# Optimization experiments

Hardware: AMD Instinct MI355X
Metric: run time of the kernel (lower is better)

The kernel has to match this reference:

```python
import jax, jax.numpy as jnp
import numpy as np

B, T, H = 16384, 64, 8
VOCABS = [2, 2, 21, 22, 5, 2, 22, 24]
EDIMS = [1, 1, 3, 3, 1, 1, 3, 3]


def _lstm_layer(xs, W_ih, W_hh, b_ih, b_hh):
    # xs: [B, T, F] -> hidden sequence [B, T, H]; torch gate order (i, f, g, o)
    Bsz = xs.shape[0]
    Hd = W_hh.shape[1]

    def step(carry, x_t):
        h, c = carry
        gates = x_t @ W_ih.T + b_ih + h @ W_hh.T + b_hh  # [B, 4H]
        i, f, g, o = jnp.split(gates, 4, axis=-1)
        c = jax.nn.sigmoid(f) * c + jax.nn.sigmoid(i) * jnp.tanh(g)
        h = jax.nn.sigmoid(o) * jnp.tanh(c)
        return (h, c), h

    init = (jnp.zeros((Bsz, Hd), xs.dtype), jnp.zeros((Bsz, Hd), xs.dtype))
    _, hs = jax.lax.scan(step, init, jnp.swapaxes(xs, 0, 1))  # scan over time
    return jnp.swapaxes(hs, 0, 1)


def setup_inputs() -> dict:
    key = jax.random.key(0)
    ks = jax.random.split(key, 40)
    cols = [jax.random.randint(ks[i], (B, T, 1), 0, VOCABS[i], dtype=jnp.int32) for i in range(8)]
    x = jnp.concatenate(cols, axis=2)  # [B, T, 8] categorical ids

    def p(k, shape):
        return jax.random.normal(k, shape, jnp.float32) * 0.1

    d = {"x": x}
    for i in range(8):
        d["e" + str(i + 1)] = p(ks[8 + i], (VOCABS[i], EDIMS[i]))
    d["W_ih0"] = p(ks[16], (4 * H, 16)); d["W_hh0"] = p(ks[17], (4 * H, H))
    d["b_ih0"] = p(ks[18], (4 * H,));   d["b_hh0"] = p(ks[19], (4 * H,))
    d["W_ih1"] = p(ks[20], (4 * H, H)); d["W_hh1"] = p(ks[21], (4 * H, H))
    d["b_ih1"] = p(ks[22], (4 * H,));   d["b_hh1"] = p(ks[23], (4 * H,))
    d["fc6_w"] = p(ks[24], (4, H)); d["fc6_b"] = p(ks[25], (4,))
    d["fc7_w"] = p(ks[26], (1, 4)); d["fc7_b"] = p(ks[27], (1,))
    d["fc1_w"] = p(ks[28], (4, H)); d["fc1_b"] = p(ks[29], (4,))
    d["fc2_w"] = p(ks[30], (1, 4)); d["fc2_b"] = p(ks[31], (1,))
    d["fc3_w"] = p(ks[32], (1, T)); d["fc3_b"] = p(ks[33], (1,))
    return d


def reference(x, e1, e2, e3, e4, e5, e6, e7, e8,
              W_ih0, W_hh0, b_ih0, b_hh0, W_ih1, W_hh1, b_ih1, b_hh1,
              fc6_w, fc6_b, fc7_w, fc7_b, fc1_w, fc1_b, fc2_w, fc2_b, fc3_w, fc3_b):
    tabs = (e1, e2, e3, e4, e5, e6, e7, e8)
    # 8-way embedding lookup + concat -> [B, T, 16]
    emb = jnp.concatenate([tabs[i][x[:, :, i]] for i in range(8)], axis=2)
    h1 = _lstm_layer(emb, W_ih0, W_hh0, b_ih0, b_hh0)
    out = _lstm_layer(h1, W_ih1, W_hh1, b_ih1, b_hh1)  # [B, T, H]
    # tiny dual FC branches applied per (b, t) position
    theta = ((out @ fc6_w.T + fc6_b) @ fc7_w.T + fc7_b)[..., 0]  # [B, T]
    h = ((out @ fc1_w.T + fc1_b) @ fc2_w.T + fc2_b)[..., 0]      # [B, T]
    pred = (theta * h) @ fc3_w.T + fc3_b  # [B, 1]
    return pred
```

## Files before the change

### kernel.cpp

```cpp
#include <hip/hip_runtime.h>
#include <hip/hip_bf16.h>

typedef float f2 __attribute__((ext_vector_type(2)));

__device__ __forceinline__ float sigf(float x) {
  return __builtin_amdgcn_rcpf(1.0f + __expf(-x));
}
__device__ __forceinline__ float tanh_fast(float x) {
  return fmaf(-2.0f, __builtin_amdgcn_rcpf(1.0f + __expf(2.0f * x)), 1.0f);
}

template<int CTRL>
__device__ __forceinline__ float dppf(float v) {
  return __builtin_bit_cast(float,
      __builtin_amdgcn_mov_dpp(__builtin_bit_cast(int, v), CTRL, 0xf, 0xf, false));
}

__device__ __forceinline__ void fanout8(float h, float* d) {
  d[0] = h;
  d[1] = dppf<0xB1>(h);
  d[2] = dppf<0x4E>(h);
  d[3] = dppf<0x1B>(h);
  float t7 = dppf<0x141>(h);
  d[7] = t7;
  d[4] = dppf<0x1B>(t7);
  d[5] = dppf<0x4E>(t7);
  d[6] = dppf<0xB1>(t7);
}

__launch_bounds__(256, 2)
__global__ void lstm_fused(
    const int* __restrict__ x,
    const float* __restrict__ e1, const float* __restrict__ e2,
    const float* __restrict__ e3, const float* __restrict__ e4,
    const float* __restrict__ e5, const float* __restrict__ e6,
    const float* __restrict__ e7, const float* __restrict__ e8,
    const float* __restrict__ W_ih0, const float* __restrict__ W_hh0,
    const float* __restrict__ b_ih0, const float* __restrict__ b_hh0,
    const float* __restrict__ W_ih1, const float* __restrict__ W_hh1,
    const float* __restrict__ b_ih1, const float* __restrict__ b_hh1,
    const float* __restrict__ fc6_w, const float* __restrict__ fc6_b,
    const float* __restrict__ fc7_w, const float* __restrict__ fc7_b,
    const float* __restrict__ fc1_w, const float* __restrict__ fc1_b,
    const float* __restrict__ fc2_w, const float* __restrict__ fc2_b,
    const float* __restrict__ fc3_w, const float* __restrict__ fc3_b,
    float* __restrict__ out)
{
  __shared__ __align__(16) float sTf[3200];
  __shared__ float sW3s[65];

  const int tid = threadIdx.x;

  {
    constexpr int RO[8]  = {0,2,4,25,47,52,54,76};
    constexpr int ED[8]  = {1,1,3,3,1,1,3,3};
    constexpr int CO[8]  = {0,1,2,5,8,9,10,13};
    constexpr int VOC[8] = {2,2,21,22,5,2,22,24};
    const float* ep[8] = {e1,e2,e3,e4,e5,e6,e7,e8};
    #pragma unroll
    for (int f = 0; f < 8; ++f) {
      const float* E = ep[f];
      for (int idx = tid; idx < VOC[f]*32; idx += 256) {
        int v = idx >> 5, m = idx & 31;
        int jj = m >> 2, q = m & 3, g = q*8 + jj;
        float s = 0.0f;
        #pragma unroll
        for (int d = 0; d < ED[f]; ++d)
          s += E[v*ED[f]+d] * W_ih0[g*16 + CO[f] + d];
        if (f == 0) s += b_ih0[g] + b_hh0[g];
        sTf[(RO[f]+v)*32 + m] = s;
      }
    }
    if (tid < 64) sW3s[tid+1] = fc3_w[tid];
    if (tid == 64) sW3s[0] = 0.f;
  }
  __syncthreads();

  const int j = tid & 7;
  const int b = (blockIdx.x << 5) + (tid >> 3);

  f2 wIF0[8], wGO0[8], iIF1[8], iGO1[8], rIF1[8], rGO1[8];
  #pragma unroll
  for (int r = 0; r < 8; ++r) {
    const int k = j ^ r;
    wIF0[r] = (f2){W_hh0[(0*8+j)*8+k], W_hh0[(1*8+j)*8+k]};
    wGO0[r] = (f2){W_hh0[(2*8+j)*8+k], W_hh0[(3*8+j)*8+k]};
    iIF1[r] = (f2){W_ih1[(0*8+j)*8+k], W_ih1[(1*8+j)*8+k]};
    iGO1[r] = (f2){W_ih1[(2*8+j)*8+k], W_ih1[(3*8+j)*8+k]};
    rIF1[r] = (f2){W_hh1[(0*8+j)*8+k], W_hh1[(1*8+j)*8+k]};
    rGO1[r] = (f2){W_hh1[(2*8+j)*8+k], W_hh1[(3*8+j)*8+k]};
  }
  const f2 bIF1 = {b_ih1[j]    + b_hh1[j],    b_ih1[8+j]  + b_hh1[8+j]};
  const f2 bGO1 = {b_ih1[16+j] + b_hh1[16+j], b_ih1[24+j] + b_hh1[24+j]};

  float f7[4], f2c[4];
  #pragma unroll
  for (int q = 0; q < 4; ++q) { f7[q] = fc7_w[q]; f2c[q] = fc2_w[q]; }
  f2 uvk[8];
  #pragma unroll
  for (int r = 0; r < 8; ++r) {
    const int k = j ^ r;
    float s1 = 0.f, s2 = 0.f;
    #pragma unroll
    for (int q = 0; q < 4; ++q) {
      s1 += f7[q]  * fc6_w[q*8+k];
      s2 += f2c[q] * fc1_w[q*8+k];
    }
    uvk[r] = (f2){s1, s2};
  }
  float cth = fc7_b[0], chh = fc2_b[0];
  #pragma unroll
  for (int q = 0; q < 4; ++q) { cth += f7[q]*fc6_b[q]; chh += f2c[q]*fc1_b[q]; }
  const f2 cc = {cth, chh};
  const float fc3b = fc3_b[0];

  float h0x[8], h1x[8];
  #pragma unroll
  for (int k = 0; k < 8; ++k) { h0x[k] = 0.f; h1x[k] = 0.f; }
  float c0 = 0.f, c1 = 0.f, acc = 0.f;

  const int4* xp = (const int4*)(x + (size_t)b * 512);
  const float4* tf4 = (const float4*)sTf;

  int4 ia = xp[0], ib = xp[1];
  float4 G0 = tf4[(      ia.x)*8 + j];
  float4 G1 = tf4[(  2 + ia.y)*8 + j];
  float4 G2 = tf4[(  4 + ia.z)*8 + j];
  float4 G3 = tf4[( 25 + ia.w)*8 + j];
  float4 G4 = tf4[( 47 + ib.x)*8 + j];
  float4 G5 = tf4[( 52 + ib.y)*8 + j];
  float4 G6 = tf4[( 54 + ib.z)*8 + j];
  float4 G7 = tf4[( 76 + ib.w)*8 + j];
  int4 na = xp[2], nb = xp[3];

  #pragma unroll 1
  for (int t = 0; t < 64; ++t) {
    const float w3p = sW3s[t];

    f2 sIFa = ((f2){G0.x,G0.y} + (f2){G1.x,G1.y}) + ((f2){G2.x,G2.y} + (f2){G3.x,G3.y});
    f2 sIFb = ((f2){G4.x,G4.y} + (f2){G5.x,G5.y}) + ((f2){G6.x,G6.y} + (f2){G7.x,G7.y});
    f2 sGOa = ((f2){G0.z,G0.w} + (f2){G1.z,G1.w}) + ((f2){G2.z,G2.w} + (f2){G3.z,G3.w});
    f2 sGOb = ((f2){G4.z,G4.w} + (f2){G5.z,G5.w}) + ((f2){G6.z,G6.w} + (f2){G7.z,G7.w});

    G0 = tf4[(      na.x)*8 + j];
    G1 = tf4[(  2 + na.y)*8 + j];
    G2 = tf4[(  4 + na.z)*8 + j];
    G3 = tf4[( 25 + na.w)*8 + j];
    G4 = tf4[( 47 + nb.x)*8 + j];
    G5 = tf4[( 52 + nb.y)*8 + j];
    G6 = tf4[( 54 + nb.z)*8 + j];
    G7 = tf4[( 76 + nb.w)*8 + j];

    {
      const int tn = (2*t + 4 <= 126) ? (2*t + 4) : 126;
      na = xp[tn]; nb = xp[tn+1];
    }

    f2 GIFa = bIF1, GIFb = (f2){0.f,0.f}, GGOa = bGO1, GGOb = (f2){0.f,0.f};
    f2 thfa = cc,  thfb = (f2){0.f,0.f};
    #pragma unroll
    for (int r = 0; r < 8; r += 2) {
      f2 hA = (f2)(h1x[r]), hB = (f2)(h1x[r+1]);
      GIFa = __builtin_elementwise_fma(rIF1[r],   hA, GIFa);
      GIFb = __builtin_elementwise_fma(rIF1[r+1], hB, GIFb);
      GGOa = __builtin_elementwise_fma(rGO1[r],   hA, GGOa);
      GGOb = __builtin_elementwise_fma(rGO1[r+1], hB, GGOb);
      thfa = __builtin_elementwise_fma(uvk[r],    hA, thfa);
      thfb = __builtin_elementwise_fma(uvk[r+1],  hB, thfb);
    }
    f2 thf = thfa + thfb;
    acc = fmaf(thf.x * thf.y, w3p, acc);

    #pragma unroll
    for (int r = 0; r < 8; r += 2) {
      sIFa = __builtin_elementwise_fma(wIF0[r],   (f2)(h0x[r]),   sIFa);
      sIFb = __builtin_elementwise_fma(wIF0[r+1], (f2)(h0x[r+1]), sIFb);
      sGOa = __builtin_elementwise_fma(wGO0[r],   (f2)(h0x[r]),   sGOa);
      sGOb = __builtin_elementwise_fma(wGO0[r+1], (f2)(h0x[r+1]), sGOb);
    }
    f2 gIF = sIFa + sIFb, gGO = sGOa + sGOb;
    float si = sigf(gIF.x), sf = sigf(gIF.y), tg = tanh_fast(gGO.x), so = sigf(gGO.y);
    c0 = fmaf(sf, c0, si * tg);
    float h0 = so * tanh_fast(c0);

    fanout8(h0, h0x);

    #pragma unroll
    for (int r = 0; r < 8; r += 2) {
      GIFa = __builtin_elementwise_fma(iIF1[r],   (f2)(h0x[r]),   GIFa);
      GIFb = __builtin_elementwise_fma(iIF1[r+1], (f2)(h0x[r+1]), GIFb);
      GGOa = __builtin_elementwise_fma(iGO1[r],   (f2)(h0x[r]),   GGOa);
      GGOb = __builtin_elementwise_fma(iGO1[r+1], (f2)(h0x[r+1]), GGOb);
    }
    f2 GIF = GIFa + GIFb, GGO = GGOa + GGOb;
    float si1 = sigf(GIF.x), sf1 = sigf(GIF.y), tg1 = tanh_fast(GGO.x), so1 = sigf(GGO.y);
    c1 = fmaf(sf1, c1, si1 * tg1);
    float h1 = so1 * tanh_fast(c1);

    fanout8(h1, h1x);
  }

  {
    f2 thfa = cc, thfb = (f2){0.f,0.f};
    #pragma unroll
    for (int r = 0; r < 8; r += 2) {
      thfa = __builtin_elementwise_fma(uvk[r],   (f2)(h1x[r]),   thfa);
      thfb = __builtin_elementwise_fma(uvk[r+1], (f2)(h1x[r+1]), thfb);
    }
    f2 thf = thfa + thfb;
    acc = fmaf(thf.x * thf.y, sW3s[64], acc);
  }

  if (j == 0) out[b] = acc + fc3b;
}

extern "C" void kernel_launch(void* const* d_in, const int* in_sizes, int n_in,
                              void* d_out, int out_size, void* d_ws, size_t ws_size,
                              hipStream_t stream) {
  const int* x = (const int*)d_in[0];
  const float *E1=(const float*)d_in[1],  *E2=(const float*)d_in[2],
              *E3=(const float*)d_in[3],  *E4=(const float*)d_in[4],
              *E5=(const float*)d_in[5],  *E6=(const float*)d_in[6],
              *E7=(const float*)d_in[7],  *E8=(const float*)d_in[8];
  const float *Wih0=(const float*)d_in[9],  *Whh0=(const float*)d_in[10],
              *bih0=(const float*)d_in[11], *bhh0=(const float*)d_in[12],
              *Wih1=(const float*)d_in[13], *Whh1=(const float*)d_in[14],
              *bih1=(const float*)d_in[15], *bhh1=(const float*)d_in[16],
              *fc6w=(const float*)d_in[17], *fc6b=(const float*)d_in[18],
              *fc7w=(const float*)d_in[19], *fc7b=(const float*)d_in[20],
              *fc1w=(const float*)d_in[21], *fc1b=(const float*)d_in[22],
              *fc2w=(const float*)d_in[23], *fc2b=(const float*)d_in[24],
              *fc3w=(const float*)d_in[25], *fc3b=(const float*)d_in[26];

  lstm_fused<<<512, 256, 0, stream>>>(
      x, E1,E2,E3,E4,E5,E6,E7,E8,
      Wih0, Whh0, bih0, bhh0, Wih1, Whh1, bih1, bhh1,
      fc6w, fc6b, fc7w, fc7b, fc1w, fc1b, fc2w, fc2b, fc3w, fc3b,
      (float*)d_out);
}
```

Baseline: 179.7 us.

## Split each LSTM row across 16 lanes with two gates per lane

Each batch row now uses 16 threads instead of 8, so each lane computes two gate pre-activations instead of four. Hidden-state broadcast moves from DPP fanout to shared-memory writes and reads. Embedding tables for paired binary features are merged into combined rows, cutting the per-step LDS lookups. The grid doubles and launch bounds allow more blocks per CU, which adds latency hiding but relies on implicit wave-synchronous LDS ordering without barriers and adds more LDS traffic per step.

```diff
diff --git a/kernel.cpp b/kernel.cpp
--- a/kernel.cpp
+++ b/kernel.cpp
@@ -9,27 +9,14 @@
 __device__ __forceinline__ float tanh_fast(float x) {
   return fmaf(-2.0f, __builtin_amdgcn_rcpf(1.0f + __expf(2.0f * x)), 1.0f);
 }
-
 template<int CTRL>
 __device__ __forceinline__ float dppf(float v) {
   return __builtin_bit_cast(float,
       __builtin_amdgcn_mov_dpp(__builtin_bit_cast(int, v), CTRL, 0xf, 0xf, false));
 }
 
-__device__ __forceinline__ void fanout8(float h, float* d) {
-  d[0] = h;
-  d[1] = dppf<0xB1>(h);
-  d[2] = dppf<0x4E>(h);
-  d[3] = dppf<0x1B>(h);
-  float t7 = dppf<0x141>(h);
-  d[7] = t7;
-  d[4] = dppf<0x1B>(t7);
-  d[5] = dppf<0x4E>(t7);
-  d[6] = dppf<0xB1>(t7);
-}
-
-__launch_bounds__(256, 2)
-__global__ void lstm_fused(
+__launch_bounds__(256, 4)
+__global__ void lstm_fused16(
     const int* __restrict__ x,
     const float* __restrict__ e1, const float* __restrict__ e2,
     const float* __restrict__ e3, const float* __restrict__ e4,
@@ -46,172 +33,197 @@
     const float* __restrict__ fc3_w, const float* __restrict__ fc3_b,
     float* __restrict__ out)
 {
-  __shared__ __align__(16) float sTf[3200];
+  __shared__ __align__(16) float sTf[103*32];
   __shared__ float sW3s[65];
+  __shared__ __align__(16) float sH0[128];
+  __shared__ __align__(16) float sH1[128];
 
   const int tid = threadIdx.x;
 
   {
-    constexpr int RO[8]  = {0,2,4,25,47,52,54,76};
-    constexpr int ED[8]  = {1,1,3,3,1,1,3,3};
-    constexpr int CO[8]  = {0,1,2,5,8,9,10,13};
-    constexpr int VOC[8] = {2,2,21,22,5,2,22,24};
-    const float* ep[8] = {e1,e2,e3,e4,e5,e6,e7,e8};
-    #pragma unroll
-    for (int f = 0; f < 8; ++f) {
-      const float* E = ep[f];
-      for (int idx = tid; idx < VOC[f]*32; idx += 256) {
-        int v = idx >> 5, m = idx & 31;
-        int jj = m >> 2, q = m & 3, g = q*8 + jj;
-        float s = 0.0f;
-        #pragma unroll
-        for (int d = 0; d < ED[f]; ++d)
-          s += E[v*ED[f]+d] * W_ih0[g*16 + CO[f] + d];
-        if (f == 0) s += b_ih0[g] + b_hh0[g];
-        sTf[(RO[f]+v)*32 + m] = s;
-      }
+    for (int idx = tid; idx < 4*32; idx += 256) {
+      int r = idx>>5, m = idx&31, L = m>>1, cg = m&1;
+      int g = ((L>>3)*2 + cg)*8 + (L&7);
+      float s = e1[r>>1]*W_ih0[g*16+0] + e2[r&1]*W_ih0[g*16+1]
+              + b_ih0[g] + b_hh0[g];
+      sTf[r*32 + m] = s;
+    }
+    for (int idx = tid; idx < 21*32; idx += 256) {
+      int r = idx>>5, m = idx&31, L = m>>1, cg = m&1;
+      int g = ((L>>3)*2 + cg)*8 + (L&7);
+      float s = 0.f;
+      #pragma unroll
+      for (int d = 0; d < 3; ++d) s += e3[r*3+d]*W_ih0[g*16+2+d];
+      sTf[(4+r)*32 + m] = s;
+    }
+    for (int idx = tid; idx < 22*32; idx += 256) {
+      int r = idx>>5, m = idx&31, L = m>>1, cg = m&1;
+      int g = ((L>>3)*2 + cg)*8 + (L&7);
+      float s = 0.f;
+      #pragma unroll
+      for (int d = 0; d < 3; ++d) s += e4[r*3+d]*W_ih0[g*16+5+d];
+      sTf[(25+r)*32 + m] = s;
+    }
+    for (int idx = tid; idx < 10*32; idx += 256) {
+      int r = idx>>5, m = idx&31, L = m>>1, cg = m&1;
+      int g = ((L>>3)*2 + cg)*8 + (L&7);
+      float s = e5[r>>1]*W_ih0[g*16+8] + e6[r&1]*W_ih0[g*16+9];
+      sTf[(47+r)*32 + m] = s;
+    }
+    for (int idx = tid; idx < 22*32; idx += 256) {
+      int r = idx>>5, m = idx&31, L = m>>1, cg = m&1;
+      int g = ((L>>3)*2 + cg)*8 + (L&7);
+      float s = 0.f;
+      #pragma unroll
+      for (int d = 0; d < 3; ++d) s += e7[r*3+d]*W_ih0[g*16+10+d];
+      sTf[(57+r)*32 + m] = s;
+    }
+    for (int idx = tid; idx < 24*32; idx += 256) {
+      int r = idx>>5, m = idx&31, L = m>>1, cg = m&1;
+      int g = ((L>>3)*2 + cg)*8 + (L&7);
+      float s = 0.f;
+      #pragma unroll
+      for (int d = 0; d < 3; ++d) s += e8[r*3+d]*W_ih0[g*16+13+d];
+      sTf[(79+r)*32 + m] = s;
     }
     if (tid < 64) sW3s[tid+1] = fc3_w[tid];
     if (tid == 64) sW3s[0] = 0.f;
   }
   __syncthreads();
 
-  const int j = tid & 7;
-  const int b = (blockIdx.x << 5) + (tid >> 3);
-
-  f2 wIF0[8], wGO0[8], iIF1[8], iGO1[8], rIF1[8], rGO1[8];
-  #pragma unroll
-  for (int r = 0; r < 8; ++r) {
-    const int k = j ^ r;
-    wIF0[r] = (f2){W_hh0[(0*8+j)*8+k], W_hh0[(1*8+j)*8+k]};
-    wGO0[r] = (f2){W_hh0[(2*8+j)*8+k], W_hh0[(3*8+j)*8+k]};
-    iIF1[r] = (f2){W_ih1[(0*8+j)*8+k], W_ih1[(1*8+j)*8+k]};
-    iGO1[r] = (f2){W_ih1[(2*8+j)*8+k], W_ih1[(3*8+j)*8+k]};
-    rIF1[r] = (f2){W_hh1[(0*8+j)*8+k], W_hh1[(1*8+j)*8+k]};
-    rGO1[r] = (f2){W_hh1[(2*8+j)*8+k], W_hh1[(3*8+j)*8+k]};
-  }
-  const f2 bIF1 = {b_ih1[j]    + b_hh1[j],    b_ih1[8+j]  + b_hh1[8+j]};
-  const f2 bGO1 = {b_ih1[16+j] + b_hh1[16+j], b_ih1[24+j] + b_hh1[24+j]};
-
+  const int lane16 = tid & 15;
+  const int j      = tid & 7;
+  const int half   = (tid >> 3) & 1;
+  const int e      = tid >> 4;
+  const int b      = (blockIdx.x << 4) + e;
+
+  const int p = (half*2)*8 + j;
+  const int q = p + 8;
+
+  f2 w0[8], i1[8], r1[8];
+  #pragma unroll
+  for (int k = 0; k < 8; ++k) {
+    w0[k] = (f2){W_hh0[p*8+k], W_hh0[q*8+k]};
+    i1[k] = (f2){W_ih1[p*8+k], W_ih1[q*8+k]};
+    r1[k] = (f2){W_hh1[p*8+k], W_hh1[q*8+k]};
+  }
+  const f2 b1 = {b_ih1[p] + b_hh1[p], b_ih1[q] + b_hh1[q]};
+
+  f2 uvk[8];
   float f7[4], f2c[4];
   #pragma unroll
-  for (int q = 0; q < 4; ++q) { f7[q] = fc7_w[q]; f2c[q] = fc2_w[q]; }
-  f2 uvk[8];
-  #pragma unroll
-  for (int r = 0; r < 8; ++r) {
-    const int k = j ^ r;
+  for (int qq = 0; qq < 4; ++qq) { f7[qq] = fc7_w[qq]; f2c[qq] = fc2_w[qq]; }
+  #pragma unroll
+  for (int k = 0; k < 8; ++k) {
     float s1 = 0.f, s2 = 0.f;
     #pragma unroll
-    for (int q = 0; q < 4; ++q) {
-      s1 += f7[q]  * fc6_w[q*8+k];
-      s2 += f2c[q] * fc1_w[q*8+k];
-    }
-    uvk[r] = (f2){s1, s2};
+    for (int qq = 0; qq < 4; ++qq) {
+      s1 += f7[qq]  * fc6_w[qq*8+k];
+      s2 += f2c[qq] * fc1_w[qq*8+k];
+    }
+    uvk[k] = (f2){s1, s2};
   }
   float cth = fc7_b[0], chh = fc2_b[0];
   #pragma unroll
-  for (int q = 0; q < 4; ++q) { cth += f7[q]*fc6_b[q]; chh += f2c[q]*fc1_b[q]; }
+  for (int qq = 0; qq < 4; ++qq) { cth += f7[qq]*fc6_b[qq]; chh += f2c[qq]*fc1_b[qq]; }
   const f2 cc = {cth, chh};
   const float fc3b = fc3_b[0];
 
+  const float aph = half ? 2.f : 1.f;
+  const float sph = half ? 2.f : 1.f;
+  const float tph = half ? -1.f : 0.f;
+
   float h0x[8], h1x[8];
   #pragma unroll
   for (int k = 0; k < 8; ++k) { h0x[k] = 0.f; h1x[k] = 0.f; }
   float c0 = 0.f, c1 = 0.f, acc = 0.f;
 
   const int4* xp = (const int4*)(x + (size_t)b * 512);
-  const float4* tf4 = (const float4*)sTf;
+  const f2* tf2 = (const f2*)sTf;
+  const float4* ph0 = (const float4*)&sH0[e*8];
+  const float4* ph1 = (const float4*)&sH1[e*8];
 
   int4 ia = xp[0], ib = xp[1];
-  float4 G0 = tf4[(      ia.x)*8 + j];
-  float4 G1 = tf4[(  2 + ia.y)*8 + j];
-  float4 G2 = tf4[(  4 + ia.z)*8 + j];
-  float4 G3 = tf4[( 25 + ia.w)*8 + j];
-  float4 G4 = tf4[( 47 + ib.x)*8 + j];
-  float4 G5 = tf4[( 52 + ib.y)*8 + j];
-  float4 G6 = tf4[( 54 + ib.z)*8 + j];
-  float4 G7 = tf4[( 76 + ib.w)*8 + j];
+  f2 G01 = tf2[(    ia.x*2 + ia.y)*16 + lane16];
+  f2 G2  = tf2[( 4 + ia.z)*16 + lane16];
+  f2 G3  = tf2[(25 + ia.w)*16 + lane16];
+  f2 G45 = tf2[(47 + ib.x*2 + ib.y)*16 + lane16];
+  f2 G6  = tf2[(57 + ib.z)*16 + lane16];
+  f2 G7  = tf2[(79 + ib.w)*16 + lane16];
   int4 na = xp[2], nb = xp[3];
 
   #pragma unroll 1
   for (int t = 0; t < 64; ++t) {
     const float w3p = sW3s[t];
 
-    f2 sIFa = ((f2){G0.x,G0.y} + (f2){G1.x,G1.y}) + ((f2){G2.x,G2.y} + (f2){G3.x,G3.y});
-    f2 sIFb = ((f2){G4.x,G4.y} + (f2){G5.x,G5.y}) + ((f2){G6.x,G6.y} + (f2){G7.x,G7.y});
-    f2 sGOa = ((f2){G0.z,G0.w} + (f2){G1.z,G1.w}) + ((f2){G2.z,G2.w} + (f2){G3.z,G3.w});
-    f2 sGOb = ((f2){G4.z,G4.w} + (f2){G5.z,G5.w}) + ((f2){G6.z,G6.w} + (f2){G7.z,G7.w});
-
-    G0 = tf4[(      na.x)*8 + j];
-    G1 = tf4[(  2 + na.y)*8 + j];
-    G2 = tf4[(  4 + na.z)*8 + j];
-    G3 = tf4[( 25 + na.w)*8 + j];
-    G4 = tf4[( 47 + nb.x)*8 + j];
-    G5 = tf4[( 52 + nb.y)*8 + j];
-    G6 = tf4[( 54 + nb.z)*8 + j];
-    G7 = tf4[( 76 + nb.w)*8 + j];
-
-    {
-      const int tn = (2*t + 4 <= 126) ? (2*t + 4) : 126;
-      na = xp[tn]; nb = xp[tn+1];
-    }
-
-    f2 GIFa = bIF1, GIFb = (f2){0.f,0.f}, GGOa = bGO1, GGOb = (f2){0.f,0.f};
-    f2 thfa = cc,  thfb = (f2){0.f,0.f};
-    #pragma unroll
-    for (int r = 0; r < 8; r += 2) {
-      f2 hA = (f2)(h1x[r]), hB = (f2)(h1x[r+1]);
-      GIFa = __builtin_elementwise_fma(rIF1[r],   hA, GIFa);
-      GIFb = __builtin_elementwise_fma(rIF1[r+1], hB, GIFb);
-      GGOa = __builtin_elementwise_fma(rGO1[r],   hA, GGOa);
-      GGOb = __builtin_elementwise_fma(rGO1[r+1], hB, GGOb);
-      thfa = __builtin_elementwise_fma(uvk[r],    hA, thfa);
-      thfb = __builtin_elementwise_fma(uvk[r+1],  hB, thfb);
-    }
-    f2 thf = thfa + thfb;
+    f2 g0 = ((G01 + G2) + (G3 + G45)) + (G6 + G7);
+
+    G01 = tf2[(    na.x*2 + na.y)*16 + lane16];
+    G2  = tf2[( 4 + na.z)*16 + lane16];
+    G3  = tf2[(25 + na.w)*16 + lane16];
+    G45 = tf2[(47 + nb.x*2 + nb.y)*16 + lane16];
+    G6  = tf2[(57 + nb.z)*16 + lane16];
+    G7  = tf2[(79 + nb.w)*16 + lane16];
+    { const int tn = (2*t + 4 <= 126) ? (2*t + 4) : 126; na = xp[tn]; nb = xp[tn+1]; }
+
+    #pragma unroll
+    for (int k = 0; k < 8; ++k)
+      g0 = __builtin_elementwise_fma(w0[k], (f2)(h0x[k]), g0);
+
+    float yp = fmaf(sph, sigf(g0.x * aph), tph);
+    float yq = sigf(g0.y);
+    float xpv = dppf<0x128>(yp);
+    float xqv = dppf<0x128>(yq);
+    float itg = yp * xpv;
+    float sfv = half ? xqv : yq;
+    float sov = half ? yq : xqv;
+    c0 = fmaf(sfv, c0, itg);
+    float h0 = sov * tanh_fast(c0);
+
+    sH0[e*8 + j] = h0;
+
+    f2 thf = cc, g1 = b1;
+    #pragma unroll
+    for (int k = 0; k < 8; ++k) {
+      f2 hb = (f2)(h1x[k]);
+      thf = __builtin_elementwise_fma(uvk[k], hb, thf);
+      g1  = __builtin_elementwise_fma(r1[k],  hb, g1);
+    }
     acc = fmaf(thf.x * thf.y, w3p, acc);
 
-    #pragma unroll
-    for (int r = 0; r < 8; r += 2) {
-      sIFa = __builtin_elementwise_fma(wIF0[r],   (f2)(h0x[r]),   sIFa);
-      sIFb = __builtin_elementwise_fma(wIF0[r+1], (f2)(h0x[r+1]), sIFb);
-      sGOa = __builtin_elementwise_fma(wGO0[r],   (f2)(h0x[r]),   sGOa);
-      sGOb = __builtin_elementwise_fma(wGO0[r+1], (f2)(h0x[r+1]), sGOb);
-    }
-    f2 gIF = sIFa + sIFb, gGO = sGOa + sGOb;
-    float si = sigf(gIF.x), sf = sigf(gIF.y), tg = tanh_fast(gGO.x), so = sigf(gGO.y);
-    c0 = fmaf(sf, c0, si * tg);
-    float h0 = so * tanh_fast(c0);
-
-    fanout8(h0, h0x);
-
-    #pragma unroll
-    for (int r = 0; r < 8; r += 2) {
-      GIFa = __builtin_elementwise_fma(iIF1[r],   (f2)(h0x[r]),   GIFa);
-      GIFb = __builtin_elementwise_fma(iIF1[r+1], (f2)(h0x[r+1]), GIFb);
-      GGOa = __builtin_elementwise_fma(iGO1[r],   (f2)(h0x[r]),   GGOa);
-      GGOb = __builtin_elementwise_fma(iGO1[r+1], (f2)(h0x[r+1]), GGOb);
-    }
-    f2 GIF = GIFa + GIFb, GGO = GGOa + GGOb;
-    float si1 = sigf(GIF.x), sf1 = sigf(GIF.y), tg1 = tanh_fast(GGO.x), so1 = sigf(GGO.y);
-    c1 = fmaf(sf1, c1, si1 * tg1);
+    { float4 lo = ph0[0], hi = ph0[1];
+      h0x[0]=lo.x; h0x[1]=lo.y; h0x[2]=lo.z; h0x[3]=lo.w;
+      h0x[4]=hi.x; h0x[5]=hi.y; h0x[6]=hi.z; h0x[7]=hi.w; }
+
+    #pragma unroll
+    for (int k = 0; k < 8; ++k)
+      g1 = __builtin_elementwise_fma(i1[k], (f2)(h0x[k]), g1);
+
+    float yp1 = fmaf(sph, sigf(g1.x * aph), tph);
+    float yq1 = sigf(g1.y);
+    float xp1 = dppf<0x128>(yp1);
+    float xq1 = dppf<0x128>(yq1);
+    float itg1 = yp1 * xp1;
+    float sf1 = half ? xq1 : yq1;
+    float so1 = half ? yq1 : xq1;
+    c1 = fmaf(sf1, c1, itg1);
     float h1 = so1 * tanh_fast(c1);
 
-    fanout8(h1, h1x);
+    sH1[e*8 + j] = h1;
+    { float4 lo = ph1[0], hi = ph1[1];
+      h1x[0]=lo.x; h1x[1]=lo.y; h1x[2]=lo.z; h1x[3]=lo.w;
+      h1x[4]=hi.x; h1x[5]=hi.y; h1x[6]=hi.z; h1x[7]=hi.w; }
   }
 
   {
-    f2 thfa = cc, thfb = (f2){0.f,0.f};
-    #pragma unroll
-    for (int r = 0; r < 8; r += 2) {
-      thfa = __builtin_elementwise_fma(uvk[r],   (f2)(h1x[r]),   thfa);
-      thfb = __builtin_elementwise_fma(uvk[r+1], (f2)(h1x[r+1]), thfb);
-    }
-    f2 thf = thfa + thfb;
+    f2 thf = cc;
+    #pragma unroll
+    for (int k = 0; k < 8; ++k)
+      thf = __builtin_elementwise_fma(uvk[k], (f2)(h1x[k]), thf);
     acc = fmaf(thf.x * thf.y, sW3s[64], acc);
   }
 
-  if (j == 0) out[b] = acc + fc3b;
+  if (lane16 == 0) out[b] = acc + fc3b;
 }
 
 extern "C" void kernel_launch(void* const* d_in, const int* in_sizes, int n_in,
@@ -232,7 +244,7 @@
               *fc2w=(const float*)d_in[23], *fc2b=(const float*)d_in[24],
               *fc3w=(const float*)d_in[25], *fc3b=(const float*)d_in[26];
 
-  lstm_fused<<<512, 256, 0, stream>>>(
+  lstm_fused16<<<1024, 256, 0, stream>>>(
       x, E1,E2,E3,E4,E5,E6,E7,E8,
       Wih0, Whh0, bih0, bhh0, Wih1, Whh1, bih1, bhh1,
       fc6w, fc6b, fc7w, fc7b, fc1w, fc1b, fc2w, fc2b, fc3w, fc3b,
```

After: 188.0 us. +4.6%, slower.
